# Optimization experiments

Hardware: AMD Instinct MI355X
Metric: run time of the kernel (lower is better)

The kernel has to match this reference:

```python
import jax, jax.numpy as jnp
import numpy as np

E = 1024  # hidden_size
H = 16    # num_heads
D = E // H  # head_dim = 64


def setup_inputs() -> dict:
    key = jax.random.key(0)
    ks = jax.random.split(key, 10)
    s = 1.0 / np.sqrt(E)
    inp = {
        "hidden_states": jax.random.normal(ks[0], (2, 2048, E), dtype=jnp.float32),
        "attention_mask": jnp.ones((2, 2048), dtype=jnp.float32),
        "Wq": jax.random.normal(ks[1], (E, E), dtype=jnp.float32) * s,
        "bq": jnp.zeros((E,), dtype=jnp.float32),
        "Wk": jax.random.normal(ks[2], (E, E), dtype=jnp.float32) * s,
        "bk": jnp.zeros((E,), dtype=jnp.float32),
        "Wv": jax.random.normal(ks[3], (E, E), dtype=jnp.float32) * s,
        "bv": jnp.zeros((E,), dtype=jnp.float32),
        "Wo": jax.random.normal(ks[4], (E, E), dtype=jnp.float32) * s,
        "bo": jnp.zeros((E,), dtype=jnp.float32),
    }
    return inp


def _split_heads(x):
    # [B, S, E] -> [B, H, S, D]
    b, s, _ = x.shape
    return x.reshape(b, s, H, D).transpose(0, 2, 1, 3)


def reference(hidden_states, attention_mask, Wq, bq, Wk, bk, Wv, bv, Wo, bo):
    b, s, _ = hidden_states.shape
    q = _split_heads(hidden_states @ Wq + bq)  # [B,H,S,D]
    k = _split_heads(hidden_states @ Wk + bk)
    v = _split_heads(hidden_states @ Wv + bv)
    scores = jnp.einsum('bhqd,bhkd->bhqk', q, k) / jnp.sqrt(jnp.float32(D))
    scores = scores + (1.0 - attention_mask)[:, None, None, :] * -10000.0
    probs = jax.nn.softmax(scores, axis=-1)
    ctx = jnp.einsum('bhqk,bhkd->bhqd', probs, v)  # [B,H,S,D]
    ctx = ctx.transpose(0, 2, 1, 3).reshape(b, s, E)
    return ctx @ Wo + bo
```

## Files before the change

### kernel.cpp

```cpp
#include <hip/hip_runtime.h>
#include <hip/hip_bf16.h>
#include <stdint.h>

typedef __bf16 bf16x8 __attribute__((ext_vector_type(8)));
typedef __bf16 bf16x4_t __attribute__((ext_vector_type(4)));
typedef float  f32x4  __attribute__((ext_vector_type(4)));
typedef float  f32x16 __attribute__((ext_vector_type(16)));
typedef short  short8 __attribute__((ext_vector_type(8)));
typedef short  short4v __attribute__((ext_vector_type(4)));
typedef float  float4v __attribute__((ext_vector_type(4)));

#define AS1 __attribute__((address_space(1)))
#define AS3 __attribute__((address_space(3)))

__device__ __forceinline__ void g2l16(const void* g, void* l) {
    __builtin_amdgcn_global_load_lds((const AS1 void*)g, (AS3 void*)l, 16, 0, 0);
}

__device__ __forceinline__ short f2bf(float f) {
    unsigned u = __builtin_bit_cast(unsigned, f);
    unsigned r = u + 0x7FFFu + ((u >> 16) & 1u);
    return (short)(r >> 16);
}

__device__ __forceinline__ bf16x8 ldb8(const short* p) {
    return __builtin_bit_cast(bf16x8, *(const short8*)p);
}

__device__ __forceinline__ float fast_exp2(float x) {
    return __builtin_amdgcn_exp2f(x);
}

#define LOG2E 1.44269504f
#define QSCL (0.125f * LOG2E)

__global__ __launch_bounds__(256) void prep(
    const float* __restrict__ X, short* __restrict__ Xb,
    const float* __restrict__ W0, const float* __restrict__ W1,
    const float* __restrict__ W2, const float* __restrict__ W3,
    short* __restrict__ T0, short* __restrict__ T1,
    short* __restrict__ T2, short* __restrict__ T3) {
    int gb = blockIdx.x;
    if (gb < 4096) {
        int i = (gb * 256 + threadIdx.x) * 4;
        float4v v = *(const float4v*)(X + i);
        short4v o;
        o[0] = f2bf(v[0]); o[1] = f2bf(v[1]); o[2] = f2bf(v[2]); o[3] = f2bf(v[3]);
        *(short4v*)(Xb + i) = o;
        return;
    }
    int t = gb - 4096;
    int z = t >> 10, rem = t & 1023;
    int xb = rem & 31, yb = rem >> 5;
    const float* W = z == 0 ? W0 : z == 1 ? W1 : z == 2 ? W2 : W3;
    short* T = z == 0 ? T0 : z == 1 ? T1 : z == 2 ? T2 : T3;
    __shared__ float tt[32][33];
    int n0 = xb * 32, k0 = yb * 32;
    int tx = threadIdx.x & 31, ty = threadIdx.x >> 5;
#pragma unroll
    for (int i = 0; i < 4; i++)
        tt[ty + i * 8][tx] = W[(size_t)(k0 + ty + i * 8) * 1024 + n0 + tx];
    __syncthreads();
#pragma unroll
    for (int i = 0; i < 4; i++)
        T[(size_t)(n0 + ty + i * 8) * 1024 + k0 + tx] = f2bf(tt[tx][ty + i * 8]);
}

#define VROW 136
__global__ __launch_bounds__(256) void gemm_qkv(
    const short* __restrict__ Xb,
    const short* __restrict__ WqT, const short* __restrict__ WkT, const short* __restrict__ WvT,
    const float* __restrict__ bq, const float* __restrict__ bk, const float* __restrict__ bv,
    short* __restrict__ Qb, short* __restrict__ Kb, short* __restrict__ VT) {
    const int K = 1024, N = 1024;
    int mt = blockIdx.x;
    int yy = blockIdx.y;
    int mat = yy >> 3, nt = yy & 7;
    const short* Bt = mat == 0 ? WqT : mat == 1 ? WkT : WvT;
    const float* bias = mat == 0 ? bq : mat == 1 ? bk : bv;

    int tid = threadIdx.x;
    int w = tid >> 6, lane = tid & 63;
    int quad = lane >> 4, l16 = lane & 15;
    int wy = w >> 1, wx = w & 1;

    __shared__ __align__(16) short smem[128 * VROW];
    short* A_lds = smem;
    short* B_lds = smem + 4096;

    f32x4 acc[4][4];
#pragma unroll
    for (int i = 0; i < 4; i++)
#pragma unroll
        for (int j = 0; j < 4; j++) acc[i][j] = (f32x4){0.f, 0.f, 0.f, 0.f};

    int m0 = mt * 128, n0 = nt * 128;

    if (mat < 2) {
        for (int kt = 0; kt < 32; kt++) {
            __syncthreads();
#pragma unroll
            for (int c = 0; c < 2; c++) {
                int row = w * 32 + c * 16 + (lane >> 2);
                g2l16(Xb + (size_t)(m0 + row) * K + kt * 32 + (lane & 3) * 8,
                      &A_lds[(w * 32 + c * 16) * 32]);
                g2l16(Bt + (size_t)(n0 + row) * K + kt * 32 + (lane & 3) * 8,
                      &B_lds[(w * 32 + c * 16) * 32]);
            }
            __syncthreads();
            bf16x8 af[4], bfr[4];
#pragma unroll
            for (int i = 0; i < 4; i++) {
                af[i]  = ldb8(&A_lds[(wy * 64 + i * 16 + l16) * 32 + quad * 8]);
                bfr[i] = ldb8(&B_lds[(wx * 64 + i * 16 + l16) * 32 + quad * 8]);
            }
#pragma unroll
            for (int ni = 0; ni < 4; ni++)
#pragma unroll
                for (int mi = 0; mi < 4; mi++)
                    acc[ni][mi] = __builtin_amdgcn_mfma_f32_16x16x32_bf16(bfr[ni], af[mi], acc[ni][mi], 0, 0, 0);
        }
        short* Cout = mat == 0 ? Qb : Kb;
        float s = mat == 0 ? QSCL : 1.0f;
#pragma unroll
        for (int ni = 0; ni < 4; ni++) {
            int c0 = n0 + wx * 64 + ni * 16 + quad * 4;
            float4v bv4 = *(const float4v*)(bias + c0);
#pragma unroll
            for (int mi = 0; mi < 4; mi++) {
                int row = m0 + wy * 64 + mi * 16 + l16;
                f32x4 a = acc[ni][mi];
                f32x4 av = {(a[0] + bv4[0]) * s, (a[1] + bv4[1]) * s,
                            (a[2] + bv4[2]) * s, (a[3] + bv4[3]) * s};
                bf16x4_t ob = __builtin_convertvector(av, bf16x4_t);
                *(short4v*)&Cout[(size_t)row * N + c0] = __builtin_bit_cast(short4v, ob);
            }
        }
    } else {
        for (int kt = 0; kt < 32; kt++) {
            __syncthreads();
#pragma unroll
            for (int c = 0; c < 2; c++) {
                int row = w * 32 + c * 16 + (lane >> 2);
                g2l16(Xb + (size_t)(m0 + row) * K + kt * 32 + (lane & 3) * 8,
                      &A_lds[(w * 32 + c * 16) * 32]);
                g2l16(Bt + (size_t)(n0 + row) * K + kt * 32 + (lane & 3) * 8,
                      &B_lds[(w * 32 + c * 16) * 32]);
            }
            __syncthreads();
            bf16x8 af[4], bfr[4];
#pragma unroll
            for (int i = 0; i < 4; i++) {
                af[i]  = ldb8(&A_lds[(wy * 64 + i * 16 + l16) * 32 + quad * 8]);
                bfr[i] = ldb8(&B_lds[(wx * 64 + i * 16 + l16) * 32 + quad * 8]);
            }
#pragma unroll
            for (int mi = 0; mi < 4; mi++)
#pragma unroll
                for (int ni = 0; ni < 4; ni++)
                    acc[mi][ni] = __builtin_amdgcn_mfma_f32_16x16x32_bf16(af[mi], bfr[ni], acc[mi][ni], 0, 0, 0);
        }
        __syncthreads();
#pragma unroll
        for (int ni = 0; ni < 4; ni++) {
            int cl = wx * 64 + ni * 16 + l16;
            float bv_ = bias[n0 + cl];
#pragma unroll
            for (int mi = 0; mi < 4; mi++) {
                int ml = wy * 64 + mi * 16 + quad * 4;
                f32x4 a = acc[mi][ni];
                f32x4 av = {a[0] + bv_, a[1] + bv_, a[2] + bv_, a[3] + bv_};
                bf16x4_t ob = __builtin_convertvector(av, bf16x4_t);
                *(short4v*)&smem[cl * VROW + ml] = __builtin_bit_cast(short4v, ob);
            }
        }
        __syncthreads();
        int bb = m0 >> 11, ss0 = m0 & 2047;
        int t16 = tid & 15, cw = tid >> 4;
#pragma unroll
        for (int p = 0; p < 8; p++) {
            int cl = p * 16 + cw;
            int col = n0 + cl;
            *(short8*)&VT[(((size_t)(bb * 16)) << 17) + (size_t)col * 2048 + ss0 + t16 * 8] =
                *(const short8*)&smem[cl * VROW + t16 * 8];
        }
    }
}

__global__ __launch_bounds__(256) void gemm_out(
    const short* __restrict__ Ab, const short* __restrict__ Bt,
    const float* __restrict__ bias, float* __restrict__ C) {
    const int K = 1024, N = 1024;
    int mt = blockIdx.x, nt = blockIdx.y;
    int tid = threadIdx.x;
    int w = tid >> 6, lane = tid & 63;
    int quad = lane >> 4, l16 = lane & 15;

    __shared__ __align__(16) short A_lds[64 * 32];
    __shared__ __align__(16) short B_lds[128 * 32];

    f32x4 acc[2][4];
#pragma unroll
    for (int ni = 0; ni < 2; ni++)
#pragma unroll
        for (int mi = 0; mi < 4; mi++) acc[ni][mi] = (f32x4){0.f, 0.f, 0.f, 0.f};

    int m0 = mt * 64, n0 = nt * 128;
    for (int kt = 0; kt < 32; kt++) {
        __syncthreads();
        {
            int row = w * 16 + (lane >> 2);
            g2l16(Ab + (size_t)(m0 + row) * K + kt * 32 + (lane & 3) * 8,
                  &A_lds[(w * 16) * 32]);
        }
#pragma unroll
        for (int c = 0; c < 2; c++) {
            int row = w * 32 + c * 16 + (lane >> 2);
            g2l16(Bt + (size_t)(n0 + row) * K + kt * 32 + (lane & 3) * 8,
                  &B_lds[(w * 32 + c * 16) * 32]);
        }
        __syncthreads();
        bf16x8 af[4], bfr[2];
#pragma unroll
        for (int i = 0; i < 4; i++)
            af[i] = ldb8(&A_lds[(i * 16 + l16) * 32 + quad * 8]);
#pragma unroll
        for (int i = 0; i < 2; i++)
            bfr[i] = ldb8(&B_lds[(w * 32 + i * 16 + l16) * 32 + quad * 8]);
#pragma unroll
        for (int ni = 0; ni < 2; ni++)
#pragma unroll
            for (int mi = 0; mi < 4; mi++)
                acc[ni][mi] = __builtin_amdgcn_mfma_f32_16x16x32_bf16(bfr[ni], af[mi], acc[ni][mi], 0, 0, 0);
    }
#pragma unroll
    for (int ni = 0; ni < 2; ni++) {
        int c0 = n0 + w * 32 + ni * 16 + quad * 4;
        float4v bv4 = *(const float4v*)(bias + c0);
#pragma unroll
        for (int mi = 0; mi < 4; mi++) {
            int row = m0 + mi * 16 + l16;
            f32x4 a = acc[ni][mi];
            float4v av = {a[0] + bv4[0], a[1] + bv4[1], a[2] + bv4[2], a[3] + bv4[3]};
            *(float4v*)&C[(size_t)row * N + c0] = av;
        }
    }
}

#define PR2 56
__global__ __launch_bounds__(512) void attn_kernel(
    const short* __restrict__ Qb, const short* __restrict__ Kb,
    const short* __restrict__ VT, const float* __restrict__ mask,
    short* __restrict__ ctx) {
    const int S = 2048, E = 1024, HH = 16;
    int g = blockIdx.x;
    int p = (g & 7) + 8 * (g >> 7);
    int qb = (g >> 3) & 15;
    int b = p >> 4, h = p & 15;

    int tid = threadIdx.x;
    int w = tid >> 6, lane = tid & 63;
    int l32 = lane & 31, hi = lane >> 5;
    int qseg = w & 3, khalf = w >> 2;

    __shared__ __align__(16) short smem_s[8192 + 8192 + 8 * 32 * PR2];
    short* K_lds = smem_s;
    short* V_lds = smem_s + 8192;
    short* Pw = smem_s + 16384 + w * 32 * PR2;
    __shared__ int maskflag;

    if (tid == 0) maskflag = 1;
    __syncthreads();
    {
        float4v m = *(const float4v*)(mask + b * S + tid * 4);
        if (!(m[0] == 1.f && m[1] == 1.f && m[2] == 1.f && m[3] == 1.f))
            maskflag = 0;
    }
    __syncthreads();
    const bool nomask = (maskflag != 0);

    int q0 = qb * 128;

    bf16x8 qf[4];
#pragma unroll
    for (int step = 0; step < 4; step++)
        qf[step] = ldb8(Qb + (size_t)(b * S + q0 + qseg * 32 + l32) * E + h * 64 + step * 16 + hi * 8);

    short8 ones_s = {0x3F80, 0x3F80, 0x3F80, 0x3F80, 0x3F80, 0x3F80, 0x3F80, 0x3F80};
    bf16x8 vones = __builtin_bit_cast(bf16x8, ones_s);

    f32x16 O_t[2];
    f32x16 lacc;
#pragma unroll
    for (int i = 0; i < 16; i++) { O_t[0][i] = 0.f; O_t[1][i] = 0.f; lacc[i] = 0.f; }

    const short* Kbase = Kb + (size_t)b * S * E + h * 64;
    const short* Vbase = VT + (size_t)(b * HH + h) * 64 * S;

    int srow = w * 8 + (lane >> 3);
    int ssrcb = (lane & 7) ^ (srow & 7);
    int l7 = lane & 7;

    g2l16(Kbase + (size_t)srow * E + ssrcb * 8, &K_lds[(w * 8) * 64]);
    g2l16(Vbase + (size_t)srow * S + 0 + ssrcb * 8, &V_lds[(w * 8) * 64]);
    __syncthreads();

    for (int kt = 0; kt < 32; kt++) {
        int cur = kt & 1;
        int k0 = kt * 64;
        if (kt < 31) {
            int k1 = k0 + 64;
            g2l16(Kbase + (size_t)(k1 + srow) * E + ssrcb * 8, &K_lds[(cur ^ 1) * 4096 + (w * 8) * 64]);
            g2l16(Vbase + (size_t)srow * S + k1 + ssrcb * 8, &V_lds[(cur ^ 1) * 4096 + (w * 8) * 64]);
        }
        const short* Kl = &K_lds[cur * 4096];
        const short* Vl = &V_lds[cur * 4096];

        f32x16 sc;
#pragma unroll
        for (int i = 0; i < 16; i++) sc[i] = 0.f;
#pragma unroll
        for (int step = 0; step < 4; step++) {
            int blk = (step * 2 + hi) ^ l7;
            bf16x8 kf = ldb8(&Kl[(khalf * 32 + l32) * 64 + blk * 8]);
            sc = __builtin_amdgcn_mfma_f32_32x32x16_bf16(kf, qf[step], sc, 0, 0, 0);
        }

        if (!nomask) {
#pragma unroll
            for (int gg = 0; gg < 4; gg++) {
                float4v mrow = *(const float4v*)(mask + b * S + k0 + khalf * 32 + gg * 8 + hi * 4);
#pragma unroll
                for (int r = 0; r < 4; r++)
                    sc[gg * 4 + r] += (1.0f - mrow[r]) * (-10000.0f * LOG2E);
            }
        }

#pragma unroll
        for (int i = 0; i < 16; i++) sc[i] = fast_exp2(sc[i]);

#pragma unroll
        for (int gg = 0; gg < 4; gg++) {
            f32x4 v4 = {sc[gg * 4 + 0], sc[gg * 4 + 1], sc[gg * 4 + 2], sc[gg * 4 + 3]};
            bf16x4_t pb = __builtin_convertvector(v4, bf16x4_t);
            *(short4v*)&Pw[l32 * PR2 + gg * 8 + hi * 4] = __builtin_bit_cast(short4v, pb);
        }

#pragma unroll
        for (int step = 0; step < 2; step++) {
            bf16x8 pf = ldb8(&Pw[l32 * PR2 + step * 16 + hi * 8]);
            lacc = __builtin_amdgcn_mfma_f32_32x32x16_bf16(vones, pf, lacc, 0, 0, 0);
#pragma unroll
            for (int dseg = 0; dseg < 2; dseg++) {
                int vblk = (khalf * 4 + step * 2 + hi) ^ l7;
                bf16x8 vf = ldb8(&Vl[(dseg * 32 + l32) * 64 + vblk * 8]);
                O_t[dseg] = __builtin_amdgcn_mfma_f32_32x32x16_bf16(vf, pf, O_t[dseg], 0, 0, 0);
            }
        }
        __syncthreads();
    }

    float* Red = (float*)smem_s;
    __syncthreads();
    if (khalf == 1) {
        float* r = &Red[(qseg * 64 + lane) * 33];
#pragma unroll
        for (int dseg = 0; dseg < 2; dseg++)
#pragma unroll
            for (int i = 0; i < 16; i++) r[dseg * 16 + i] = O_t[dseg][i];
        r[32] = lacc[0];
    }
    __syncthreads();
    if (khalf == 0) {
        const float* r = &Red[(qseg * 64 + lane) * 33];
        float l = lacc[0] + r[32];
        float inv = l > 0.f ? 1.0f / l : 0.f;
        int row = q0 + qseg * 32 + l32;
#pragma unroll
        for (int dseg = 0; dseg < 2; dseg++) {
#pragma unroll
            for (int gg = 0; gg < 4; gg++) {
                f32x4 v4 = {(O_t[dseg][gg * 4 + 0] + r[dseg * 16 + gg * 4 + 0]) * inv,
                            (O_t[dseg][gg * 4 + 1] + r[dseg * 16 + gg * 4 + 1]) * inv,
                            (O_t[dseg][gg * 4 + 2] + r[dseg * 16 + gg * 4 + 2]) * inv,
                            (O_t[dseg][gg * 4 + 3] + r[dseg * 16 + gg * 4 + 3]) * inv};
                bf16x4_t ob = __builtin_convertvector(v4, bf16x4_t);
                *(short4v*)&ctx[(size_t)(b * S + row) * E + h * 64 + dseg * 32 + gg * 8 + hi * 4] =
                    __builtin_bit_cast(short4v, ob);
            }
        }
    }
}

extern "C" void kernel_launch(void* const* d_in, const int* in_sizes, int n_in,
                              void* d_out, int out_size, void* d_ws, size_t ws_size,
                              hipStream_t stream) {
    const float* X    = (const float*)d_in[0];
    const float* mask = (const float*)d_in[1];
    const float* Wq   = (const float*)d_in[2];
    const float* bq   = (const float*)d_in[3];
    const float* Wk   = (const float*)d_in[4];
    const float* bk   = (const float*)d_in[5];
    const float* Wv   = (const float*)d_in[6];
    const float* bv   = (const float*)d_in[7];
    const float* Wo   = (const float*)d_in[8];
    const float* bo   = (const float*)d_in[9];
    float* out = (float*)d_out;

    char* ws = (char*)d_ws;
    short* Xb  = (short*)(ws);
    short* WqT = (short*)(ws + (8u << 20));
    short* WkT = (short*)(ws + (10u << 20));
    short* WvT = (short*)(ws + (12u << 20));
    short* WoT = (short*)(ws + (14u << 20));
    short* Qb  = (short*)(ws + (16u << 20));
    short* Kb  = (short*)(ws + (24u << 20));
    short* VT  = (short*)(ws + (32u << 20));
    short* ctx = Xb;

    prep<<<8192, 256, 0, stream>>>(X, Xb, Wq, Wk, Wv, Wo, WqT, WkT, WvT, WoT);
    gemm_qkv<<<dim3(32, 24), 256, 0, stream>>>(Xb, WqT, WkT, WvT, bq, bk, bv, Qb, Kb, VT);
    attn_kernel<<<512, 512, 0, stream>>>(Qb, Kb, VT, mask, ctx);
    gemm_out<<<dim3(64, 8), 256, 0, stream>>>(ctx, WoT, bo, out);
}
```

Baseline: 196.1 us.

## Double-buffer LDS tiles in QKV and output GEMMs, pad attention P rows

Both projection GEMMs now use two LDS buffers: the next K-tile is fetched with global_load_lds while MFMAs run on the current tile, and each iteration has one barrier instead of two. This aims to hide global load latency behind compute. Separately, the attention P-tile row pitch goes from 56 to 60 shorts and is read as two 8-byte loads, a layout change meant to cut LDS bank conflicts. There is no explicit vmcnt wait before the barrier, so correctness depends on the barrier waiting for outstanding async LDS loads. The larger LDS footprint may also lower occupancy.

```diff
diff --git a/kernel.cpp b/kernel.cpp
--- a/kernel.cpp
+++ b/kernel.cpp
@@ -85,8 +85,6 @@
     int wy = w >> 1, wx = w & 1;
 
     __shared__ __align__(16) short smem[128 * VROW];
-    short* A_lds = smem;
-    short* B_lds = smem + 4096;
 
     f32x4 acc[4][4];
 #pragma unroll
@@ -95,30 +93,40 @@
         for (int j = 0; j < 4; j++) acc[i][j] = (f32x4){0.f, 0.f, 0.f, 0.f};
 
     int m0 = mt * 128, n0 = nt * 128;
+
+    auto stage = [&](int kt, short* A, short* B) {
+#pragma unroll
+        for (int c = 0; c < 2; c++) {
+            int row = w * 32 + c * 16 + (lane >> 2);
+            g2l16(Xb + (size_t)(m0 + row) * K + kt * 32 + (lane & 3) * 8,
+                  &A[(w * 32 + c * 16) * 32]);
+            g2l16(Bt + (size_t)(n0 + row) * K + kt * 32 + (lane & 3) * 8,
+                  &B[(w * 32 + c * 16) * 32]);
+        }
+    };
+
+    stage(0, smem, smem + 8192);
+    __syncthreads();
 
     if (mat < 2) {
         for (int kt = 0; kt < 32; kt++) {
-            __syncthreads();
-#pragma unroll
-            for (int c = 0; c < 2; c++) {
-                int row = w * 32 + c * 16 + (lane >> 2);
-                g2l16(Xb + (size_t)(m0 + row) * K + kt * 32 + (lane & 3) * 8,
-                      &A_lds[(w * 32 + c * 16) * 32]);
-                g2l16(Bt + (size_t)(n0 + row) * K + kt * 32 + (lane & 3) * 8,
-                      &B_lds[(w * 32 + c * 16) * 32]);
-            }
-            __syncthreads();
+            int cur = kt & 1;
+            const short* Al = cur ? smem + 4096 : smem;
+            const short* Bl = cur ? smem + 12288 : smem + 8192;
+            if (kt < 31)
+                stage(kt + 1, cur ? smem : smem + 4096, cur ? smem + 8192 : smem + 12288);
             bf16x8 af[4], bfr[4];
 #pragma unroll
             for (int i = 0; i < 4; i++) {
-                af[i]  = ldb8(&A_lds[(wy * 64 + i * 16 + l16) * 32 + quad * 8]);
-                bfr[i] = ldb8(&B_lds[(wx * 64 + i * 16 + l16) * 32 + quad * 8]);
+                af[i]  = ldb8(&Al[(wy * 64 + i * 16 + l16) * 32 + quad * 8]);
+                bfr[i] = ldb8(&Bl[(wx * 64 + i * 16 + l16) * 32 + quad * 8]);
             }
 #pragma unroll
             for (int ni = 0; ni < 4; ni++)
 #pragma unroll
                 for (int mi = 0; mi < 4; mi++)
                     acc[ni][mi] = __builtin_amdgcn_mfma_f32_16x16x32_bf16(bfr[ni], af[mi], acc[ni][mi], 0, 0, 0);
+            __syncthreads();
         }
         short* Cout = mat == 0 ? Qb : Kb;
         float s = mat == 0 ? QSCL : 1.0f;
@@ -138,29 +146,24 @@
         }
     } else {
         for (int kt = 0; kt < 32; kt++) {
-            __syncthreads();
-#pragma unroll
-            for (int c = 0; c < 2; c++) {
-                int row = w * 32 + c * 16 + (lane >> 2);
-                g2l16(Xb + (size_t)(m0 + row) * K + kt * 32 + (lane & 3) * 8,
-                      &A_lds[(w * 32 + c * 16) * 32]);
-                g2l16(Bt + (size_t)(n0 + row) * K + kt * 32 + (lane & 3) * 8,
-                      &B_lds[(w * 32 + c * 16) * 32]);
-            }
-            __syncthreads();
+            int cur = kt & 1;
+            const short* Al = cur ? smem + 4096 : smem;
+            const short* Bl = cur ? smem + 12288 : smem + 8192;
+            if (kt < 31)
+                stage(kt + 1, cur ? smem : smem + 4096, cur ? smem + 8192 : smem + 12288);
             bf16x8 af[4], bfr[4];
 #pragma unroll
             for (int i = 0; i < 4; i++) {
-                af[i]  = ldb8(&A_lds[(wy * 64 + i * 16 + l16) * 32 + quad * 8]);
-                bfr[i] = ldb8(&B_lds[(wx * 64 + i * 16 + l16) * 32 + quad * 8]);
+                af[i]  = ldb8(&Al[(wy * 64 + i * 16 + l16) * 32 + quad * 8]);
+                bfr[i] = ldb8(&Bl[(wx * 64 + i * 16 + l16) * 32 + quad * 8]);
             }
 #pragma unroll
             for (int mi = 0; mi < 4; mi++)
 #pragma unroll
                 for (int ni = 0; ni < 4; ni++)
                     acc[mi][ni] = __builtin_amdgcn_mfma_f32_16x16x32_bf16(af[mi], bfr[ni], acc[mi][ni], 0, 0, 0);
-        }
-        __syncthreads();
+            __syncthreads();
+        }
 #pragma unroll
         for (int ni = 0; ni < 4; ni++) {
             int cl = wx * 64 + ni * 16 + l16;
@@ -196,8 +199,7 @@
     int w = tid >> 6, lane = tid & 63;
     int quad = lane >> 4, l16 = lane & 15;
 
-    __shared__ __align__(16) short A_lds[64 * 32];
-    __shared__ __align__(16) short B_lds[128 * 32];
+    __shared__ __align__(16) short smem[12288];
 
     f32x4 acc[2][4];
 #pragma unroll
@@ -206,32 +208,43 @@
         for (int mi = 0; mi < 4; mi++) acc[ni][mi] = (f32x4){0.f, 0.f, 0.f, 0.f};
 
     int m0 = mt * 64, n0 = nt * 128;
-    for (int kt = 0; kt < 32; kt++) {
-        __syncthreads();
+
+    auto stage = [&](int kt, short* A, short* B) {
         {
             int row = w * 16 + (lane >> 2);
             g2l16(Ab + (size_t)(m0 + row) * K + kt * 32 + (lane & 3) * 8,
-                  &A_lds[(w * 16) * 32]);
+                  &A[(w * 16) * 32]);
         }
 #pragma unroll
         for (int c = 0; c < 2; c++) {
             int row = w * 32 + c * 16 + (lane >> 2);
             g2l16(Bt + (size_t)(n0 + row) * K + kt * 32 + (lane & 3) * 8,
-                  &B_lds[(w * 32 + c * 16) * 32]);
-        }
-        __syncthreads();
+                  &B[(w * 32 + c * 16) * 32]);
+        }
+    };
+
+    stage(0, smem, smem + 4096);
+    __syncthreads();
+
+    for (int kt = 0; kt < 32; kt++) {
+        int cur = kt & 1;
+        const short* Al = cur ? smem + 2048 : smem;
+        const short* Bl = cur ? smem + 8192 : smem + 4096;
+        if (kt < 31)
+            stage(kt + 1, cur ? smem : smem + 2048, cur ? smem + 4096 : smem + 8192);
         bf16x8 af[4], bfr[2];
 #pragma unroll
         for (int i = 0; i < 4; i++)
-            af[i] = ldb8(&A_lds[(i * 16 + l16) * 32 + quad * 8]);
+            af[i] = ldb8(&Al[(i * 16 + l16) * 32 + quad * 8]);
 #pragma unroll
         for (int i = 0; i < 2; i++)
-            bfr[i] = ldb8(&B_lds[(w * 32 + i * 16 + l16) * 32 + quad * 8]);
+            bfr[i] = ldb8(&Bl[(w * 32 + i * 16 + l16) * 32 + quad * 8]);
 #pragma unroll
         for (int ni = 0; ni < 2; ni++)
 #pragma unroll
             for (int mi = 0; mi < 4; mi++)
                 acc[ni][mi] = __builtin_amdgcn_mfma_f32_16x16x32_bf16(bfr[ni], af[mi], acc[ni][mi], 0, 0, 0);
+        __syncthreads();
     }
 #pragma unroll
     for (int ni = 0; ni < 2; ni++) {
@@ -247,7 +260,7 @@
     }
 }
 
-#define PR2 56
+#define PR2 60
 __global__ __launch_bounds__(512) void attn_kernel(
     const short* __restrict__ Qb, const short* __restrict__ Kb,
     const short* __restrict__ VT, const float* __restrict__ mask,
@@ -348,7 +361,10 @@
 
 #pragma unroll
         for (int step = 0; step < 2; step++) {
-            bf16x8 pf = ldb8(&Pw[l32 * PR2 + step * 16 + hi * 8]);
+            short4v p0 = *(const short4v*)&Pw[l32 * PR2 + step * 16 + hi * 8];
+            short4v p1 = *(const short4v*)&Pw[l32 * PR2 + step * 16 + hi * 8 + 4];
+            short8 pc = {p0[0], p0[1], p0[2], p0[3], p1[0], p1[1], p1[2], p1[3]};
+            bf16x8 pf = __builtin_bit_cast(bf16x8, pc);
             lacc = __builtin_amdgcn_mfma_f32_32x32x16_bf16(vones, pf, lacc, 0, 0, 0);
 #pragma unroll
             for (int dseg = 0; dseg < 2; dseg++) {
```

Result: no change. 194.5 us (-0.8%).
